# Optimization experiments

Hardware: AMD Instinct MI355X
Metric: run time of the kernel (lower is better)

The kernel has to match this reference:

```python
import jax, jax.numpy as jnp
import numpy as np

N_NODES = 100000
N_EDGES = 1600000
NFEAT, NHID, NCLASS = 128, 64, 10
N_LAYERS = 5


def setup_inputs() -> dict:
    key = jax.random.key(0)
    ks = jax.random.split(key, 4 + 2 * N_LAYERS)
    x = jax.random.normal(ks[0], (N_NODES, NFEAT), dtype=jnp.float32)
    edge_src = jax.random.randint(ks[1], (N_EDGES,), 0, N_NODES, dtype=jnp.int32)
    edge_dst = jax.random.randint(ks[2], (N_EDGES,), 0, N_NODES, dtype=jnp.int32)
    edge_w = jax.random.uniform(ks[3], (N_EDGES,), dtype=jnp.float32)
    dims = [NFEAT] + [NHID] * (N_LAYERS - 1) + [NCLASS]
    inp = {"x": x, "edge_src": edge_src, "edge_dst": edge_dst, "edge_w": edge_w}
    for i in range(N_LAYERS):
        din, dout = dims[i], dims[i + 1]
        s = 1.0 / np.sqrt(din)
        inp[f"W{i}"] = jax.random.uniform(ks[4 + 2 * i], (din, dout), minval=-s, maxval=s, dtype=jnp.float32)
        inp[f"b{i}"] = jax.random.uniform(ks[5 + 2 * i], (dout,), minval=-s, maxval=s, dtype=jnp.float32)
    return inp


def _gcn_layer(h, src, dst, w, W, b):
    # linear projection then weighted gather-scatter aggregation (DGL u_mul_e + sum)
    h = h @ W + b                      # [N, dout]
    m = h[src] * w[:, None]            # [E, dout] messages
    return jax.ops.segment_sum(m, dst, num_segments=N_NODES)


def reference(x, edge_src, edge_dst, edge_w, W0, b0, W1, b1, W2, b2, W3, b3, W4, b4):
    Ws = [W0, W1, W2, W3, W4]
    bs = [b0, b1, b2, b3, b4]
    h = x
    for i in range(N_LAYERS - 1):
        h = _gcn_layer(h, edge_src, edge_dst, edge_w, Ws[i], bs[i])
        h = jax.nn.relu(h)  # dropout is identity in eval mode
    h = _gcn_layer(h, edge_src, edge_dst, edge_w, Ws[-1], bs[-1])
    return h  # [N, nclass]; .squeeze(1) is a no-op for nclass>1
```

## Files before the change

### kernel.cpp

```cpp
#include <hip/hip_runtime.h>
#include <hip/hip_bf16.h>

#define N_NODES 100000
#define N_EDGES 1600000

__global__ void hist_kernel(const int* __restrict__ dst, int* __restrict__ deg, int E) {
    int gid = blockIdx.x * blockDim.x + threadIdx.x;
    if (gid < E) atomicAdd(&deg[dst[gid]], 1);
}

__global__ void scan1(const int* __restrict__ deg, int* __restrict__ row_ptr,
                      int* __restrict__ partials, int N) {
    __shared__ int sh[1024];
    int gid = blockIdx.x * 1024 + threadIdx.x;
    int v = (gid < N) ? deg[gid] : 0;
    sh[threadIdx.x] = v;
    __syncthreads();
    for (int off = 1; off < 1024; off <<= 1) {
        int t = (threadIdx.x >= off) ? sh[threadIdx.x - off] : 0;
        __syncthreads();
        sh[threadIdx.x] += t;
        __syncthreads();
    }
    if (gid < N) row_ptr[gid] = sh[threadIdx.x] - v;
    if (threadIdx.x == 1023) partials[blockIdx.x] = sh[1023];
}

__global__ void scan2(int* __restrict__ partials, int nb) {
    __shared__ int sh[128];
    int v = (threadIdx.x < nb) ? partials[threadIdx.x] : 0;
    sh[threadIdx.x] = v;
    __syncthreads();
    for (int off = 1; off < 128; off <<= 1) {
        int t = (threadIdx.x >= off) ? sh[threadIdx.x - off] : 0;
        __syncthreads();
        sh[threadIdx.x] += t;
        __syncthreads();
    }
    if (threadIdx.x < nb) partials[threadIdx.x] = sh[threadIdx.x] - v;
}

__global__ void scan3(int* __restrict__ row_ptr, int* __restrict__ cursor,
                      const int* __restrict__ partials, int N, int E) {
    int gid = blockIdx.x * 1024 + threadIdx.x;
    if (gid < N) {
        int r = row_ptr[gid] + partials[blockIdx.x];
        row_ptr[gid] = r;
        cursor[gid] = r;
    }
    if (gid == 0) row_ptr[N] = E;
}

__global__ void place_kernel(const int* __restrict__ src, const int* __restrict__ dst,
                             const float* __restrict__ w, int* __restrict__ cursor,
                             int2* __restrict__ csr, int E) {
    int gid = blockIdx.x * blockDim.x + threadIdx.x;
    if (gid < E) {
        int d = dst[gid];
        int pos = atomicAdd(&cursor[d], 1);
        csr[pos] = make_int2(src[gid], __float_as_int(w[gid]));
    }
}

__global__ __launch_bounds__(256) void gemm0(const float* __restrict__ X,
                                             const float* __restrict__ W,
                                             const float* __restrict__ b,
                                             float* __restrict__ P, int N) {
    __shared__ float Ws[128 * 64];
    for (int i = threadIdx.x; i < 128 * 64 / 4; i += blockDim.x)
        ((float4*)Ws)[i] = ((const float4*)W)[i];
    __syncthreads();

    int tid = blockIdx.x * blockDim.x + threadIdx.x;
    int cg = (tid & 3) * 16;
    int row0 = (tid >> 2) * 4;
    if (row0 >= N) return;

    float acc[4][16];
#pragma unroll
    for (int c = 0; c < 16; ++c) {
        float bc = b[cg + c];
#pragma unroll
        for (int r = 0; r < 4; ++r) acc[r][c] = bc;
    }

    for (int k0 = 0; k0 < 128; k0 += 4) {
        float4 xv[4];
#pragma unroll
        for (int r = 0; r < 4; ++r)
            xv[r] = *(const float4*)&X[(long)(row0 + r) * 128 + k0];
#pragma unroll
        for (int kk = 0; kk < 4; ++kk) {
            const float* wr = &Ws[(k0 + kk) * 64 + cg];
            float4 w0 = *(const float4*)&wr[0];
            float4 w1 = *(const float4*)&wr[4];
            float4 w2 = *(const float4*)&wr[8];
            float4 w3 = *(const float4*)&wr[12];
#pragma unroll
            for (int r = 0; r < 4; ++r) {
                float x = (&xv[r].x)[kk];
                acc[r][0]  = fmaf(x, w0.x, acc[r][0]);  acc[r][1]  = fmaf(x, w0.y, acc[r][1]);
                acc[r][2]  = fmaf(x, w0.z, acc[r][2]);  acc[r][3]  = fmaf(x, w0.w, acc[r][3]);
                acc[r][4]  = fmaf(x, w1.x, acc[r][4]);  acc[r][5]  = fmaf(x, w1.y, acc[r][5]);
                acc[r][6]  = fmaf(x, w1.z, acc[r][6]);  acc[r][7]  = fmaf(x, w1.w, acc[r][7]);
                acc[r][8]  = fmaf(x, w2.x, acc[r][8]);  acc[r][9]  = fmaf(x, w2.y, acc[r][9]);
                acc[r][10] = fmaf(x, w2.z, acc[r][10]); acc[r][11] = fmaf(x, w2.w, acc[r][11]);
                acc[r][12] = fmaf(x, w3.x, acc[r][12]); acc[r][13] = fmaf(x, w3.y, acc[r][13]);
                acc[r][14] = fmaf(x, w3.z, acc[r][14]); acc[r][15] = fmaf(x, w3.w, acc[r][15]);
            }
        }
    }
#pragma unroll
    for (int r = 0; r < 4; ++r)
#pragma unroll
        for (int c4 = 0; c4 < 4; ++c4)
            *(float4*)&P[(long)(row0 + r) * 64 + cg + c4 * 4] =
                make_float4(acc[r][c4 * 4], acc[r][c4 * 4 + 1], acc[r][c4 * 4 + 2], acc[r][c4 * 4 + 3]);
}

template <int DIN, int DOUT, bool RELU>
__global__ void gemm4(const float* __restrict__ H, const float* __restrict__ W,
                      const float* __restrict__ b, float* __restrict__ out, int N) {
    __shared__ float Ws[DIN * DOUT];
    for (int i = threadIdx.x; i < DIN * DOUT / 4; i += blockDim.x)
        ((float4*)Ws)[i] = ((const float4*)W)[i];
    __syncthreads();

    int gid = blockIdx.x * blockDim.x + threadIdx.x;
    int row = gid / (DOUT / 4);
    int cg = (gid - row * (DOUT / 4)) * 4;
    if (row >= N) return;

    const float* h = H + (long)row * DIN;
    float4 acc = *(const float4*)&b[cg];
#pragma unroll
    for (int k0 = 0; k0 < DIN; k0 += 4) {
        float4 hv = *(const float4*)&h[k0];
        if (RELU) {
            hv.x = fmaxf(hv.x, 0.f); hv.y = fmaxf(hv.y, 0.f);
            hv.z = fmaxf(hv.z, 0.f); hv.w = fmaxf(hv.w, 0.f);
        }
#pragma unroll
        for (int kk = 0; kk < 4; ++kk) {
            float x = (&hv.x)[kk];
            float4 wv = *(const float4*)&Ws[(k0 + kk) * DOUT + cg];
            acc.x = fmaf(x, wv.x, acc.x); acc.y = fmaf(x, wv.y, acc.y);
            acc.z = fmaf(x, wv.z, acc.z); acc.w = fmaf(x, wv.w, acc.w);
        }
    }
    *(float4*)&out[(long)row * DOUT + cg] = acc;
}

__global__ void gemm_last(const float* __restrict__ H, const float* __restrict__ W,
                          const float* __restrict__ b, float* __restrict__ out, int N) {
    __shared__ float Ws[64 * 10];
    for (int i = threadIdx.x; i < 64 * 10; i += blockDim.x) Ws[i] = W[i];
    __syncthreads();
    int gid = blockIdx.x * blockDim.x + threadIdx.x;
    int row = gid / 10;
    int col = gid - row * 10;
    if (row >= N) return;
    const float* h = H + (long)row * 64;
    float acc = b[col];
#pragma unroll
    for (int k = 0; k < 64; ++k)
        acc = fmaf(fmaxf(h[k], 0.f), Ws[k * 10 + col], acc);
    out[(long)row * 16 + col] = acc;
}

__global__ __launch_bounds__(256) void agg64v2(const float* __restrict__ P,
                                               const int2* __restrict__ csr,
                                               const int* __restrict__ row_ptr,
                                               float* __restrict__ A, int N) {
    int lane = threadIdx.x & 63;
    int half = lane >> 5;
    int fl = (lane & 31) * 2;
    long gw = ((long)blockIdx.x * blockDim.x + threadIdx.x) >> 6;
    int n = (int)(gw * 2) + half;
    if (n >= N) return;
    int beg = row_ptr[n], end = row_ptr[n + 1];

    float ax = 0.f, ay = 0.f;
    int j = beg;
    for (; j + 3 < end; j += 4) {
        int2 e0 = csr[j], e1 = csr[j + 1], e2 = csr[j + 2], e3 = csr[j + 3];
        float2 v0 = *(const float2*)&P[(size_t)((unsigned)e0.x * 64u + fl)];
        float2 v1 = *(const float2*)&P[(size_t)((unsigned)e1.x * 64u + fl)];
        float2 v2 = *(const float2*)&P[(size_t)((unsigned)e2.x * 64u + fl)];
        float2 v3 = *(const float2*)&P[(size_t)((unsigned)e3.x * 64u + fl)];
        float w0 = __int_as_float(e0.y), w1 = __int_as_float(e1.y);
        float w2 = __int_as_float(e2.y), w3 = __int_as_float(e3.y);
        ax = fmaf(w0, v0.x, ax); ay = fmaf(w0, v0.y, ay);
        ax = fmaf(w1, v1.x, ax); ay = fmaf(w1, v1.y, ay);
        ax = fmaf(w2, v2.x, ax); ay = fmaf(w2, v2.y, ay);
        ax = fmaf(w3, v3.x, ax); ay = fmaf(w3, v3.y, ay);
    }
    for (; j < end; ++j) {
        int2 e = csr[j];
        float2 v = *(const float2*)&P[(size_t)((unsigned)e.x * 64u + fl)];
        float w = __int_as_float(e.y);
        ax = fmaf(w, v.x, ax); ay = fmaf(w, v.y, ay);
    }
    *(float2*)&A[(size_t)n * 64 + fl] = make_float2(ax, ay);
}

__global__ __launch_bounds__(256) void agg10v2(const float* __restrict__ P,
                                               const int2* __restrict__ csr,
                                               const int* __restrict__ row_ptr,
                                               float* __restrict__ out, int N) {
    int lane = threadIdx.x & 63;
    int g  = lane >> 3;
    int sl = lane & 7;
    long gw = ((long)blockIdx.x * blockDim.x + threadIdx.x) >> 6;
    if (gw >= N) return;
    int n = (int)gw;
    int beg = row_ptr[n], end = row_ptr[n + 1];

    float ax = 0.f, ay = 0.f;
    for (int j0 = beg; j0 < end; j0 += 8) {
        int j = j0 + g;
        if (j < end && sl < 5) {
            int2 e = csr[j];
            float2 v = *(const float2*)&P[(size_t)((unsigned)e.x * 16u + sl * 2)];
            float w = __int_as_float(e.y);
            ax = fmaf(w, v.x, ax); ay = fmaf(w, v.y, ay);
        }
    }
#pragma unroll
    for (int m = 8; m <= 32; m <<= 1) {
        ax += __shfl_xor(ax, m);
        ay += __shfl_xor(ay, m);
    }
    if (g == 0 && sl < 5)
        *(float2*)&out[(size_t)n * 10 + sl * 2] = make_float2(ax, ay);
}

extern "C" void kernel_launch(void* const* d_in, const int* in_sizes, int n_in,
                              void* d_out, int out_size, void* d_ws, size_t ws_size,
                              hipStream_t stream) {
    const float* x        = (const float*)d_in[0];
    const int*   edge_src = (const int*)d_in[1];
    const int*   edge_dst = (const int*)d_in[2];
    const float* edge_w   = (const float*)d_in[3];
    const float* W0 = (const float*)d_in[4];   const float* b0 = (const float*)d_in[5];
    const float* W1 = (const float*)d_in[6];   const float* b1 = (const float*)d_in[7];
    const float* W2 = (const float*)d_in[8];   const float* b2 = (const float*)d_in[9];
    const float* W3 = (const float*)d_in[10];  const float* b3 = (const float*)d_in[11];
    const float* W4 = (const float*)d_in[12];  const float* b4 = (const float*)d_in[13];
    float* out = (float*)d_out;

    char* p = (char*)d_ws;
    auto take = [&](size_t bytes) { char* r = p; p += (bytes + 255) & ~(size_t)255; return r; };
    float* B0       = (float*)take((size_t)N_NODES * 64 * sizeof(float));
    float* B1       = (float*)take((size_t)N_NODES * 64 * sizeof(float));
    int2*  csr      = (int2*) take((size_t)N_EDGES * sizeof(int2));
    int*   deg      = (int*)  take((size_t)N_NODES * sizeof(int));
    int*   row_ptr  = (int*)  take((size_t)(N_NODES + 1) * sizeof(int));
    int*   cursor   = (int*)  take((size_t)N_NODES * sizeof(int));
    int*   partials = (int*)  take(1024 * sizeof(int));

    const int NB = (N_NODES + 1023) / 1024;
    const int EB = (N_EDGES + 255) / 256;

    hipMemsetAsync(deg, 0, (size_t)N_NODES * sizeof(int), stream);
    hist_kernel<<<EB, 256, 0, stream>>>(edge_dst, deg, N_EDGES);
    scan1<<<NB, 1024, 0, stream>>>(deg, row_ptr, partials, N_NODES);
    scan2<<<1, 128, 0, stream>>>(partials, NB);
    scan3<<<NB, 1024, 0, stream>>>(row_ptr, cursor, partials, N_NODES, N_EDGES);
    place_kernel<<<EB, 256, 0, stream>>>(edge_src, edge_dst, edge_w, cursor, csr, N_EDGES);

    gemm0<<<(N_NODES + 255) / 256, 256, 0, stream>>>(x, W0, b0, B0, N_NODES);

    const int AGG2_BLOCKS = (((N_NODES + 1) / 2) * 64 + 255) / 256;
    const int G4_BLOCKS = (N_NODES * 16 + 255) / 256;

    agg64v2<<<AGG2_BLOCKS, 256, 0, stream>>>(B0, csr, row_ptr, B1, N_NODES);
    gemm4<64, 64, true><<<G4_BLOCKS, 256, 0, stream>>>(B1, W1, b1, B0, N_NODES);
    agg64v2<<<AGG2_BLOCKS, 256, 0, stream>>>(B0, csr, row_ptr, B1, N_NODES);
    gemm4<64, 64, true><<<G4_BLOCKS, 256, 0, stream>>>(B1, W2, b2, B0, N_NODES);
    agg64v2<<<AGG2_BLOCKS, 256, 0, stream>>>(B0, csr, row_ptr, B1, N_NODES);
    gemm4<64, 64, true><<<G4_BLOCKS, 256, 0, stream>>>(B1, W3, b3, B0, N_NODES);
    agg64v2<<<AGG2_BLOCKS, 256, 0, stream>>>(B0, csr, row_ptr, B1, N_NODES);

    gemm_last<<<(N_NODES * 10 + 255) / 256, 256, 0, stream>>>(B1, W4, b4, B0, N_NODES);
    agg10v2<<<(N_NODES * 64 + 255) / 256, 256, 0, stream>>>(B0, csr, row_ptr, out, N_NODES);
}
```

Measured before the change: 709.5 us.

## Build CSR with two-pass bucketed placement to localize scatter writes

Replaces the single global-atomic CSR placement with a two-stage scheme. Edges are first scattered into buckets of 128 destination nodes, with the local node index packed into the high bits of src. A per-bucket block then places each edge at its final position using atomics in shared memory. This aims to cut the cost of random 8-byte scattered writes and contended global atomics over 100k cursors, at the price of an extra pass through a temporary buffer that reuses the B1 feature buffer.

```diff
diff --git a/kernel.cpp b/kernel.cpp
--- a/kernel.cpp
+++ b/kernel.cpp
@@ -3,6 +3,9 @@
 
 #define N_NODES 100000
 #define N_EDGES 1600000
+#define BKT_SHIFT 7
+#define BKT_NODES 128
+#define NBKT ((N_NODES + BKT_NODES - 1) / BKT_NODES)
 
 __global__ void hist_kernel(const int* __restrict__ dst, int* __restrict__ deg, int E) {
     int gid = blockIdx.x * blockDim.x + threadIdx.x;
@@ -40,25 +43,50 @@
     if (threadIdx.x < nb) partials[threadIdx.x] = sh[threadIdx.x] - v;
 }
 
-__global__ void scan3(int* __restrict__ row_ptr, int* __restrict__ cursor,
-                      const int* __restrict__ partials, int N, int E) {
+__global__ void scan3(int* __restrict__ row_ptr, const int* __restrict__ partials,
+                      int N, int E) {
     int gid = blockIdx.x * 1024 + threadIdx.x;
-    if (gid < N) {
-        int r = row_ptr[gid] + partials[blockIdx.x];
-        row_ptr[gid] = r;
-        cursor[gid] = r;
-    }
+    if (gid < N) row_ptr[gid] += partials[blockIdx.x];
     if (gid == 0) row_ptr[N] = E;
 }
 
-__global__ void place_kernel(const int* __restrict__ src, const int* __restrict__ dst,
-                             const float* __restrict__ w, int* __restrict__ cursor,
-                             int2* __restrict__ csr, int E) {
+__global__ void init_bcur(const int* __restrict__ row_ptr, int* __restrict__ bcur) {
+    int b = threadIdx.x + blockIdx.x * blockDim.x;
+    if (b < NBKT) bcur[b] = row_ptr[b * BKT_NODES];
+}
+
+__global__ void place_bucket(const int* __restrict__ src, const int* __restrict__ dst,
+                             const float* __restrict__ w, int* __restrict__ bcur,
+                             int2* __restrict__ tmp, int E) {
     int gid = blockIdx.x * blockDim.x + threadIdx.x;
     if (gid < E) {
         int d = dst[gid];
-        int pos = atomicAdd(&cursor[d], 1);
-        csr[pos] = make_int2(src[gid], __float_as_int(w[gid]));
+        int b = d >> BKT_SHIFT;
+        int pos = atomicAdd(&bcur[b], 1);
+        tmp[pos] = make_int2(((d & (BKT_NODES - 1)) << 17) | src[gid],
+                             __float_as_int(w[gid]));
+    }
+}
+
+__global__ __launch_bounds__(256) void place_local(const int2* __restrict__ tmp,
+                                                   const int* __restrict__ row_ptr,
+                                                   int2* __restrict__ csr) {
+    __shared__ int lcur[BKT_NODES];
+    int b = blockIdx.x;
+    int node0 = b * BKT_NODES;
+    if (threadIdx.x < BKT_NODES) {
+        int node = node0 + threadIdx.x;
+        lcur[threadIdx.x] = (node < N_NODES) ? row_ptr[node] : N_EDGES;
+    }
+    __syncthreads();
+    int ebeg = row_ptr[node0];
+    int nend = node0 + BKT_NODES; if (nend > N_NODES) nend = N_NODES;
+    int eend = row_ptr[nend];
+    for (int t = ebeg + threadIdx.x; t < eend; t += 256) {
+        int2 e = tmp[t];
+        int nl = e.x >> 17;
+        int pos = atomicAdd(&lcur[nl], 1);
+        csr[pos] = make_int2(e.x & 0x1FFFF, e.y);
     }
 }
 
@@ -252,12 +280,13 @@
     char* p = (char*)d_ws;
     auto take = [&](size_t bytes) { char* r = p; p += (bytes + 255) & ~(size_t)255; return r; };
     float* B0       = (float*)take((size_t)N_NODES * 64 * sizeof(float));
-    float* B1       = (float*)take((size_t)N_NODES * 64 * sizeof(float));
+    float* B1f      = (float*)take((size_t)N_NODES * 64 * sizeof(float));
     int2*  csr      = (int2*) take((size_t)N_EDGES * sizeof(int2));
     int*   deg      = (int*)  take((size_t)N_NODES * sizeof(int));
     int*   row_ptr  = (int*)  take((size_t)(N_NODES + 1) * sizeof(int));
-    int*   cursor   = (int*)  take((size_t)N_NODES * sizeof(int));
+    int*   bcur     = (int*)  take((size_t)NBKT * sizeof(int));
     int*   partials = (int*)  take(1024 * sizeof(int));
+    int2* tmp = (int2*)B1f;
 
     const int NB = (N_NODES + 1023) / 1024;
     const int EB = (N_EDGES + 255) / 256;
@@ -266,22 +295,24 @@
     hist_kernel<<<EB, 256, 0, stream>>>(edge_dst, deg, N_EDGES);
     scan1<<<NB, 1024, 0, stream>>>(deg, row_ptr, partials, N_NODES);
     scan2<<<1, 128, 0, stream>>>(partials, NB);
-    scan3<<<NB, 1024, 0, stream>>>(row_ptr, cursor, partials, N_NODES, N_EDGES);
-    place_kernel<<<EB, 256, 0, stream>>>(edge_src, edge_dst, edge_w, cursor, csr, N_EDGES);
+    scan3<<<NB, 1024, 0, stream>>>(row_ptr, partials, N_NODES, N_EDGES);
+    init_bcur<<<(NBKT + 255) / 256, 256, 0, stream>>>(row_ptr, bcur);
+    place_bucket<<<EB, 256, 0, stream>>>(edge_src, edge_dst, edge_w, bcur, tmp, N_EDGES);
+    place_local<<<NBKT, 256, 0, stream>>>(tmp, row_ptr, csr);
 
     gemm0<<<(N_NODES + 255) / 256, 256, 0, stream>>>(x, W0, b0, B0, N_NODES);
 
     const int AGG2_BLOCKS = (((N_NODES + 1) / 2) * 64 + 255) / 256;
     const int G4_BLOCKS = (N_NODES * 16 + 255) / 256;
 
-    agg64v2<<<AGG2_BLOCKS, 256, 0, stream>>>(B0, csr, row_ptr, B1, N_NODES);
-    gemm4<64, 64, true><<<G4_BLOCKS, 256, 0, stream>>>(B1, W1, b1, B0, N_NODES);
-    agg64v2<<<AGG2_BLOCKS, 256, 0, stream>>>(B0, csr, row_ptr, B1, N_NODES);
-    gemm4<64, 64, true><<<G4_BLOCKS, 256, 0, stream>>>(B1, W2, b2, B0, N_NODES);
-    agg64v2<<<AGG2_BLOCKS, 256, 0, stream>>>(B0, csr, row_ptr, B1, N_NODES);
-    gemm4<64, 64, true><<<G4_BLOCKS, 256, 0, stream>>>(B1, W3, b3, B0, N_NODES);
-    agg64v2<<<AGG2_BLOCKS, 256, 0, stream>>>(B0, csr, row_ptr, B1, N_NODES);
-
-    gemm_last<<<(N_NODES * 10 + 255) / 256, 256, 0, stream>>>(B1, W4, b4, B0, N_NODES);
+    agg64v2<<<AGG2_BLOCKS, 256, 0, stream>>>(B0, csr, row_ptr, B1f, N_NODES);
+    gemm4<64, 64, true><<<G4_BLOCKS, 256, 0, stream>>>(B1f, W1, b1, B0, N_NODES);
+    agg64v2<<<AGG2_BLOCKS, 256, 0, stream>>>(B0, csr, row_ptr, B1f, N_NODES);
+    gemm4<64, 64, true><<<G4_BLOCKS, 256, 0, stream>>>(B1f, W2, b2, B0, N_NODES);
+    agg64v2<<<AGG2_BLOCKS, 256, 0, stream>>>(B0, csr, row_ptr, B1f, N_NODES);
+    gemm4<64, 64, true><<<G4_BLOCKS, 256, 0, stream>>>(B1f, W3, b3, B0, N_NODES);
+    agg64v2<<<AGG2_BLOCKS, 256, 0, stream>>>(B0, csr, row_ptr, B1f, N_NODES);
+
+    gemm_last<<<(N_NODES * 10 + 255) / 256, 256, 0, stream>>>(B1f, W4, b4, B0, N_NODES);
     agg10v2<<<(N_NODES * 64 + 255) / 256, 256, 0, stream>>>(B0, csr, row_ptr, out, N_NODES);
 }
```

Result: slower. 983.7 us (+38.6%).
